# Kernel optimization log

Hardware: AMD Instinct MI355X
Metric: run time of the kernel (lower is better)

Reference implementation:

```python
import jax, jax.numpy as jnp
import numpy as np

NIN, NOUT = 256, 64

def setup_inputs() -> dict:
    key = jax.random.key(0)
    k1, k2, k3, k4 = jax.random.split(key, 4)
    B, T = 4, 4096
    y = jax.random.normal(k1, (B, T, NIN), dtype=jnp.float32)
    # torch Linear(nin, nout).weight has shape [nout, nin]; store as [nin, nout]
    s = 1.0 / np.sqrt(NIN)
    Wq = jax.random.uniform(k2, (NIN, NOUT), jnp.float32, -s, s)
    Wk = jax.random.uniform(k3, (NIN, NOUT), jnp.float32, -s, s)
    Wv = jax.random.uniform(k4, (NIN, NOUT), jnp.float32, -s, s)
    return {"y": y, "Wq": Wq, "Wk": Wk, "Wv": Wv}

def reference(y, Wq, Wk, Wv):
    T = y.shape[1]
    que = y @ Wq  # [B,T,NOUT]
    key = y @ Wk
    val = y @ Wv
    att = jnp.einsum('bqd,bkd->bqk', que, key)  # [B,T,T]
    causal = jnp.tril(jnp.ones((T, T), dtype=bool))  # True = keep
    att = jnp.where(causal, att, -jnp.inf)
    att = jax.nn.softmax(att / jnp.sqrt(jnp.float32(NOUT)), axis=-1)
    return jnp.einsum('bqk,bkd->bqd', att, val)
```

## Files before the change

### kernel.cpp

```cpp
#include <hip/hip_runtime.h>
#include <hip/hip_bf16.h>

#define TLEN 4096
#define NINP 256
#define DD   64

#define QSCALE 0.18033688011112042f

typedef __attribute__((ext_vector_type(8))) short bf16x8;
typedef __attribute__((ext_vector_type(4))) short bf16x4;
typedef __attribute__((ext_vector_type(4))) float f32x4;

union U8 { bf16x8 v; uint u[4]; };
union U4 { bf16x4 v; uint u[2]; };

__device__ inline ushort bfu(float x) {
    union { float f; uint u; } a; a.f = x;
    uint r = a.u + 0x7fffu + ((a.u >> 16) & 1u);
    return (ushort)(r >> 16);
}
__device__ inline uint pk2(float lo, float hi) {
    return (uint)bfu(lo) | ((uint)bfu(hi) << 16);
}
__device__ inline uint cvtpk(float lo, float hi) {
    uint r;
    asm("v_cvt_pk_bf16_f32 %0, %1, %2" : "=v"(r) : "v"(lo), "v"(hi));
    return r;
}

__device__ inline bf16x8 ld16(const ushort* p) {
    return *(const bf16x8*)p;
}
__device__ inline bf16x8 ld8x2(const ushort* p) {
    U8 u;
    uint2 a = *(const uint2*)p;
    uint2 b = *(const uint2*)(p + 4);
    u.u[0] = a.x; u.u[1] = a.y; u.u[2] = b.x; u.u[3] = b.y;
    return u.v;
}

__global__ __launch_bounds__(256) void prep_wt(
    const float* __restrict__ Wq, const float* __restrict__ Wk,
    const float* __restrict__ Wv, ushort* __restrict__ WT)
{
    __shared__ ushort lt[256 * 66];
    const int t = threadIdx.x;
    const int m = blockIdx.x;
    const float* W = (m == 0) ? Wq : ((m == 1) ? Wk : Wv);
    const float scale = (m == 0) ? QSCALE : 1.0f;

    #pragma unroll
    for (int j = 0; j < 16; ++j) {
        int i4 = t + 256 * j;
        float4 v = *(const float4*)&W[i4 * 4];
        int k = i4 >> 4, d = (i4 * 4) & 63;
        *(uint*)&lt[k * 66 + d]     = pk2(v.x * scale, v.y * scale);
        *(uint*)&lt[k * 66 + d + 2] = pk2(v.z * scale, v.w * scale);
    }
    __syncthreads();
    #pragma unroll
    for (int j = 0; j < 32; ++j) {
        int o2 = t + 256 * j;
        int d = o2 >> 7, k = (o2 & 127) * 2;
        uint pk = (uint)lt[k * 66 + d] | ((uint)lt[(k + 1) * 66 + d] << 16);
        *(uint*)&WT[m * 16384 + d * 256 + k] = pk;
    }
}

__global__ __launch_bounds__(256, 3) void qkv_kernel(
    const float* __restrict__ y, const ushort* __restrict__ WT,
    ushort* __restrict__ Qh, ushort* __restrict__ Kp, ushort* __restrict__ Vp,
    const int rbn)
{
    __shared__ ushort Wl[64 * 268];
    __shared__ ushort tb[64 * 68];

    const int t = threadIdx.x;
    const int w = t >> 6, lane = t & 63;
    const int quad = lane >> 4, l15 = lane & 15;
    const int mb = blockIdx.x / rbn;
    const int rb = blockIdx.x % rbn;
    const int rowbase = rb * 64;
    const int myrow = rowbase + w * 16 + l15;

    {
        int n = t >> 2, seg = t & 3;
        const ushort* src = WT + mb * 16384 + n * 256 + seg * 64;
        ushort* dst = &Wl[n * 268 + seg * 64];
        #pragma unroll
        for (int j = 0; j < 16; ++j)
            ((uint2*)dst)[j] = ((const uint2*)src)[j];
    }

    bf16x8 afrag[8];
    const float* yrow = y + (size_t)myrow * NINP;
    #pragma unroll
    for (int s = 0; s < 8; ++s) {
        float4 lo = *(const float4*)&yrow[s * 32 + quad * 8];
        float4 hi = *(const float4*)&yrow[s * 32 + quad * 8 + 4];
        U8 u;
        u.u[0] = pk2(lo.x, lo.y);
        u.u[1] = pk2(lo.z, lo.w);
        u.u[2] = pk2(hi.x, hi.y);
        u.u[3] = pk2(hi.z, hi.w);
        afrag[s] = u.v;
    }

    __syncthreads();

    f32x4 acc[4];
    #pragma unroll
    for (int nt = 0; nt < 4; ++nt) acc[nt] = f32x4{0.f, 0.f, 0.f, 0.f};

    #pragma unroll
    for (int s = 0; s < 8; ++s)
        #pragma unroll
        for (int nt = 0; nt < 4; ++nt) {
            bf16x8 bfrag = ld8x2(&Wl[(nt * 16 + l15) * 268 + s * 32 + quad * 8]);
            acc[nt] = __builtin_amdgcn_mfma_f32_16x16x32_bf16(
                afrag[s], bfrag, acc[nt], 0, 0, 0);
        }

    if (mb == 0) {
        #pragma unroll
        for (int nt = 0; nt < 4; ++nt)
            #pragma unroll
            for (int r = 0; r < 4; ++r)
                tb[(w * 16 + quad * 4 + r) * 68 + nt * 16 + l15] = bfu(acc[nt][r]);
        __syncthreads();
        int row = t >> 2, seg = t & 3;
        ushort* gd = Qh + (size_t)(rowbase + row) * DD + seg * 16;
        const ushort* sp = &tb[row * 68 + seg * 16];
        #pragma unroll
        for (int j = 0; j < 4; ++j) ((uint2*)gd)[j] = ((const uint2*)sp)[j];
    } else if (mb == 1) {
        #pragma unroll
        for (int nt = 0; nt < 4; ++nt)
            #pragma unroll
            for (int r = 0; r < 4; ++r)
                tb[(w * 16 + quad * 4 + r) * 68 + nt * 16 + l15] = bfu(acc[nt][r]);
        __syncthreads();
        #pragma unroll
        for (int j = 0; j < 2; ++j) {
            int idx = t + 256 * j;
            int instr = idx >> 6, ln = idx & 63;
            int kt = instr >> 1, s = instr & 1;
            int q2 = ln >> 4, l15b = ln & 15;
            int row = kt * 16 + l15b, dcol = s * 32 + q2 * 8;
            const ushort* sp = &tb[row * 68 + dcol];
            ushort* gd = Kp + (size_t)rb * 4096 + idx * 8;
            ((uint2*)gd)[0] = ((const uint2*)sp)[0];
            ((uint2*)gd)[1] = ((const uint2*)sp)[1];
        }
    } else {
        #pragma unroll
        for (int nt = 0; nt < 4; ++nt) {
            int d = nt * 16 + l15;
            #pragma unroll
            for (int r = 0; r < 4; r += 2) {
                int tt = w * 16 + quad * 4 + r;
                *(uint*)&tb[d * 68 + tt] = pk2(acc[nt][r], acc[nt][r + 1]);
            }
        }
        __syncthreads();
        #pragma unroll
        for (int j = 0; j < 2; ++j) {
            int idx = t + 256 * j;
            int instr = idx >> 6, ln = idx & 63;
            int nt = instr >> 1, m = instr & 1;
            int q2 = ln >> 4, l15b = ln & 15;
            int d = nt * 16 + l15b;
            int k0 = 32 * m + q2 * 4;
            ushort* gd = Vp + (size_t)rb * 4096 + idx * 8;
            ((uint2*)gd)[0] = *(const uint2*)&tb[d * 68 + k0];
            ((uint2*)gd)[1] = *(const uint2*)&tb[d * 68 + k0 + 16];
        }
    }
}

__device__ inline void load_k32(bf16x8 (&kf)[2][2], const ushort* __restrict__ Kw,
                                int ci)
{
    const ushort* base = Kw + (size_t)ci * 2048;
    #pragma unroll
    for (int kt = 0; kt < 2; ++kt)
        #pragma unroll
        for (int s = 0; s < 2; ++s)
            kf[kt][s] = ld16(base + (kt * 2 + s) * 512);
}

__device__ inline void load_v32(U4 (&vt)[4][2], const ushort* __restrict__ Vw,
                                int ci)
{
    const ushort* base = Vw + (size_t)(ci >> 1) * 4096 + (ci & 1) * 512;
    #pragma unroll
    for (int nt = 0; nt < 4; ++nt) {
        U8 uu; uu.v = ld16(base + nt * 1024);
        vt[nt][0].u[0] = uu.u[0]; vt[nt][0].u[1] = uu.u[1];
        vt[nt][1].u[0] = uu.u[2]; vt[nt][1].u[1] = uu.u[3];
    }
}

__global__ __launch_bounds__(768, 2) void attn_kernel(
    const ushort* __restrict__ Qh, const ushort* __restrict__ Kp,
    const ushort* __restrict__ Vp, float* __restrict__ out)
{
    __shared__ float Ob[12][32 * 68];
    __shared__ float lb[12][32];

    const int t = threadIdx.x;
    const int w = t >> 6, lane = t & 63;
    const int quad = lane >> 4, l15 = lane & 15;

    const int x  = blockIdx.x & 7;
    const int b  = x >> 1;
    const int pr = (((int)blockIdx.x >> 3) << 1) | (x & 1);

    const ushort* Qb = Qh + (size_t)b * TLEN * DD;
    const ushort* Kw = Kp + (size_t)b * 64 * 4096 + lane * 8;
    const ushort* Vw = Vp + (size_t)b * 64 * 4096 + lane * 8;
    float* outb = out + (size_t)b * TLEN * DD;

    for (int half = 0; half < 2; ++half) {
        const int tile = half ? (127 - pr) : pr;
        const int seg  = half ? (11 - w) : w;
        const int qb   = tile * 32;
        const int nc   = tile + 1;
        const int cps  = (nc + 11) / 12;
        const int clo  = seg * cps;
        const int chi  = (nc < clo + cps) ? nc : (clo + cps);

        f32x4 oT[2][4];
        #pragma unroll
        for (int qt = 0; qt < 2; ++qt)
            #pragma unroll
            for (int nt = 0; nt < 4; ++nt)
                oT[qt][nt] = f32x4{0.f, 0.f, 0.f, 0.f};
        float l_acc[2] = {0.f, 0.f};

        if (clo < chi) {
            bf16x8 qf[2][2];
            #pragma unroll
            for (int qt = 0; qt < 2; ++qt)
                #pragma unroll
                for (int s = 0; s < 2; ++s)
                    qf[qt][s] = ld16(Qb + (size_t)(qb + qt * 16 + l15) * DD + s * 32 + quad * 8);

            bf16x8 kf[2][2];
            load_k32(kf, Kw, clo);

            for (int ci = clo; ci < chi; ++ci) {
                const int c0 = ci * 32;

                U4 vt[4][2];
                load_v32(vt, Vw, ci);

                f32x4 st[2][2];
                #pragma unroll
                for (int qt = 0; qt < 2; ++qt)
                    #pragma unroll
                    for (int kt = 0; kt < 2; ++kt)
                        st[qt][kt] = f32x4{0.f, 0.f, 0.f, 0.f};
                __builtin_amdgcn_s_setprio(1);
                #pragma unroll
                for (int s = 0; s < 2; ++s)
                    #pragma unroll
                    for (int qt = 0; qt < 2; ++qt)
                        #pragma unroll
                        for (int kt = 0; kt < 2; ++kt)
                            st[qt][kt] = __builtin_amdgcn_mfma_f32_16x16x32_bf16(
                                kf[kt][s], qf[qt][s], st[qt][kt], 0, 0, 0);
                __builtin_amdgcn_s_setprio(0);

                if (ci + 1 < chi) load_k32(kf, Kw, ci + 1);

                U4 pa[2][2];
                if (c0 + 31 <= qb) {
                    #pragma unroll
                    for (int qt = 0; qt < 2; ++qt)
                        #pragma unroll
                        for (int kt = 0; kt < 2; ++kt) {
                            float p0 = exp2f(st[qt][kt][0]);
                            float p1 = exp2f(st[qt][kt][1]);
                            float p2 = exp2f(st[qt][kt][2]);
                            float p3 = exp2f(st[qt][kt][3]);
                            l_acc[qt] += (p0 + p1) + (p2 + p3);
                            pa[qt][kt].u[0] = cvtpk(p0, p1);
                            pa[qt][kt].u[1] = cvtpk(p2, p3);
                        }
                } else {
                    #pragma unroll
                    for (int qt = 0; qt < 2; ++qt) {
                        const int q = qb + qt * 16 + l15;
                        #pragma unroll
                        for (int kt = 0; kt < 2; ++kt) {
                            const int kb0 = c0 + kt * 16 + quad * 4;
                            float p[4];
                            #pragma unroll
                            for (int r = 0; r < 4; ++r) {
                                float e = exp2f(st[qt][kt][r]);
                                p[r] = (kb0 + r <= q) ? e : 0.f;
                                l_acc[qt] += p[r];
                            }
                            pa[qt][kt].u[0] = cvtpk(p[0], p[1]);
                            pa[qt][kt].u[1] = cvtpk(p[2], p[3]);
                        }
                    }
                }

                __builtin_amdgcn_s_setprio(1);
                #pragma unroll
                for (int qt = 0; qt < 2; ++qt)
                    #pragma unroll
                    for (int nt = 0; nt < 4; ++nt)
                        #pragma unroll
                        for (int kt = 0; kt < 2; ++kt)
                            oT[qt][nt] = __builtin_amdgcn_mfma_f32_16x16x16bf16_1k(
                                vt[nt][kt].v, pa[qt][kt].v, oT[qt][nt], 0, 0, 0);
                __builtin_amdgcn_s_setprio(0);
            }

            #pragma unroll
            for (int qt = 0; qt < 2; ++qt) {
                l_acc[qt] += __shfl_xor(l_acc[qt], 16, 64);
                l_acc[qt] += __shfl_xor(l_acc[qt], 32, 64);
            }
        }

        #pragma unroll
        for (int qt = 0; qt < 2; ++qt) {
            #pragma unroll
            for (int nt = 0; nt < 4; ++nt)
                #pragma unroll
                for (int r = 0; r < 4; ++r)
                    Ob[w][(qt * 16 + l15) * 68 + nt * 16 + quad * 4 + r] = oT[qt][nt][r];
            if (quad == 0) lb[w][qt * 16 + l15] = l_acc[qt];
        }
        __syncthreads();

        #pragma unroll
        for (int e = 0; e < 3; ++e) {
            int idx = t + 768 * e;
            if (idx < 2048) {
                int q = idx >> 6, d = idx & 63;
                float s = 0.f, ls = 0.f;
                #pragma unroll
                for (int ww = 0; ww < 12; ++ww) {
                    s += Ob[ww][q * 68 + d];
                    ls += lb[ww][q];
                }
                outb[(size_t)(qb + q) * DD + d] = s * __builtin_amdgcn_rcpf(ls);
            }
        }
        __syncthreads();
    }
}

extern "C" void kernel_launch(void* const* d_in, const int* in_sizes, int n_in,
                              void* d_out, int out_size, void* d_ws, size_t ws_size,
                              hipStream_t stream) {
    const float* y  = (const float*)d_in[0];
    const float* Wq = (const float*)d_in[1];
    const float* Wk = (const float*)d_in[2];
    const float* Wv = (const float*)d_in[3];
    float* outp = (float*)d_out;

    const int rows = in_sizes[0] / NINP;
    const int nb = rows / TLEN;
    const int rbn = rows / 64;

    ushort* WT = (ushort*)d_ws;
    ushort* Qh = WT + 3 * 16384;
    ushort* Kp = Qh + (size_t)rows * DD;
    ushort* Vp = Kp + (size_t)rows * DD;

    prep_wt<<<3, 256, 0, stream>>>(Wq, Wk, Wv, WT);
    qkv_kernel<<<3 * rbn, 256, 0, stream>>>(y, WT, Qh, Kp, Vp, rbn);
    attn_kernel<<<nb * 64, 768, 0, stream>>>(Qh, Kp, Vp, outp);
}
```

Baseline: 101.4 us.

## Prefetch K two chunks ahead and load QKV weights pre-swizzled from global

prep_wt now writes the projection weights directly in MFMA B-fragment order. qkv_kernel can therefore load each fragment with one 16-byte global read, dropping the LDS staging buffer and its barrier. The attention inner loop is split into a helper that alternates two K register buffers, prefetching K two chunks ahead to hide load latency. The attention launch bound is raised to 3 blocks per CU. That caps registers more tightly and may cause spills, while the LDS footprint likely still allows only two resident blocks.

New measurement: 101.1 us, median of 2. Within noise of the previous version (-0.3%).

```diff
diff --git a/kernel.cpp b/kernel.cpp
--- a/kernel.cpp
+++ b/kernel.cpp
@@ -31,17 +31,10 @@
 __device__ inline bf16x8 ld16(const ushort* p) {
     return *(const bf16x8*)p;
 }
-__device__ inline bf16x8 ld8x2(const ushort* p) {
-    U8 u;
-    uint2 a = *(const uint2*)p;
-    uint2 b = *(const uint2*)(p + 4);
-    u.u[0] = a.x; u.u[1] = a.y; u.u[2] = b.x; u.u[3] = b.y;
-    return u.v;
-}
 
 __global__ __launch_bounds__(256) void prep_wt(
     const float* __restrict__ Wq, const float* __restrict__ Wk,
-    const float* __restrict__ Wv, ushort* __restrict__ WT)
+    const float* __restrict__ Wv, ushort* __restrict__ WTf)
 {
     __shared__ ushort lt[256 * 66];
     const int t = threadIdx.x;
@@ -59,20 +52,27 @@
     }
     __syncthreads();
     #pragma unroll
-    for (int j = 0; j < 32; ++j) {
-        int o2 = t + 256 * j;
-        int d = o2 >> 7, k = (o2 & 127) * 2;
-        uint pk = (uint)lt[k * 66 + d] | ((uint)lt[(k + 1) * 66 + d] << 16);
-        *(uint*)&WT[m * 16384 + d * 256 + k] = pk;
-    }
-}
-
-__global__ __launch_bounds__(256, 3) void qkv_kernel(
-    const float* __restrict__ y, const ushort* __restrict__ WT,
+    for (int j = 0; j < 8; ++j) {
+        int slot = t + 256 * j;
+        int u = slot >> 6, ln = slot & 63;
+        int s = u >> 2, nt = u & 3;
+        int d = nt * 16 + (ln & 15);
+        int k0 = s * 32 + (ln >> 4) * 8;
+        uint a0 = (uint)lt[(k0 + 0) * 66 + d] | ((uint)lt[(k0 + 1) * 66 + d] << 16);
+        uint a1 = (uint)lt[(k0 + 2) * 66 + d] | ((uint)lt[(k0 + 3) * 66 + d] << 16);
+        uint a2 = (uint)lt[(k0 + 4) * 66 + d] | ((uint)lt[(k0 + 5) * 66 + d] << 16);
+        uint a3 = (uint)lt[(k0 + 6) * 66 + d] | ((uint)lt[(k0 + 7) * 66 + d] << 16);
+        ushort* gd = WTf + m * 16384 + slot * 8;
+        ((uint2*)gd)[0] = uint2{a0, a1};
+        ((uint2*)gd)[1] = uint2{a2, a3};
+    }
+}
+
+__global__ __launch_bounds__(256) void qkv_kernel(
+    const float* __restrict__ y, const ushort* __restrict__ WTf,
     ushort* __restrict__ Qh, ushort* __restrict__ Kp, ushort* __restrict__ Vp,
     const int rbn)
 {
-    __shared__ ushort Wl[64 * 268];
     __shared__ ushort tb[64 * 68];
 
     const int t = threadIdx.x;
@@ -82,15 +82,6 @@
     const int rb = blockIdx.x % rbn;
     const int rowbase = rb * 64;
     const int myrow = rowbase + w * 16 + l15;
-
-    {
-        int n = t >> 2, seg = t & 3;
-        const ushort* src = WT + mb * 16384 + n * 256 + seg * 64;
-        ushort* dst = &Wl[n * 268 + seg * 64];
-        #pragma unroll
-        for (int j = 0; j < 16; ++j)
-            ((uint2*)dst)[j] = ((const uint2*)src)[j];
-    }
 
     bf16x8 afrag[8];
     const float* yrow = y + (size_t)myrow * NINP;
@@ -106,17 +97,16 @@
         afrag[s] = u.v;
     }
 
-    __syncthreads();
-
     f32x4 acc[4];
     #pragma unroll
     for (int nt = 0; nt < 4; ++nt) acc[nt] = f32x4{0.f, 0.f, 0.f, 0.f};
 
+    const ushort* Wm = WTf + mb * 16384 + lane * 8;
     #pragma unroll
     for (int s = 0; s < 8; ++s)
         #pragma unroll
         for (int nt = 0; nt < 4; ++nt) {
-            bf16x8 bfrag = ld8x2(&Wl[(nt * 16 + l15) * 268 + s * 32 + quad * 8]);
+            bf16x8 bfrag = ld16(Wm + (s * 4 + nt) * 512);
             acc[nt] = __builtin_amdgcn_mfma_f32_16x16x32_bf16(
                 afrag[s], bfrag, acc[nt], 0, 0, 0);
         }
@@ -201,7 +191,82 @@
     }
 }
 
-__global__ __launch_bounds__(768, 2) void attn_kernel(
+__device__ inline void chunk32(
+    const bf16x8 (&kf)[2][2], bf16x8 (&kfn)[2][2],
+    const ushort* __restrict__ Kw, const ushort* __restrict__ Vw,
+    const bf16x8 (&qf)[2][2], f32x4 (&oT)[2][4], float (&l_acc)[2],
+    int ci, int pf, int chi, int qb, int quad, int l15)
+{
+    const int c0 = ci * 32;
+    U4 vt[4][2];
+    load_v32(vt, Vw, ci);
+
+    f32x4 st[2][2];
+    #pragma unroll
+    for (int qt = 0; qt < 2; ++qt)
+        #pragma unroll
+        for (int kt = 0; kt < 2; ++kt)
+            st[qt][kt] = f32x4{0.f, 0.f, 0.f, 0.f};
+    __builtin_amdgcn_s_setprio(1);
+    #pragma unroll
+    for (int s = 0; s < 2; ++s)
+        #pragma unroll
+        for (int qt = 0; qt < 2; ++qt)
+            #pragma unroll
+            for (int kt = 0; kt < 2; ++kt)
+                st[qt][kt] = __builtin_amdgcn_mfma_f32_16x16x32_bf16(
+                    kf[kt][s], qf[qt][s], st[qt][kt], 0, 0, 0);
+    __builtin_amdgcn_s_setprio(0);
+
+    if (pf < chi) load_k32(kfn, Kw, pf);
+
+    U4 pa[2][2];
+    if (c0 + 31 <= qb) {
+        #pragma unroll
+        for (int qt = 0; qt < 2; ++qt)
+            #pragma unroll
+            for (int kt = 0; kt < 2; ++kt) {
+                float p0 = exp2f(st[qt][kt][0]);
+                float p1 = exp2f(st[qt][kt][1]);
+                float p2 = exp2f(st[qt][kt][2]);
+                float p3 = exp2f(st[qt][kt][3]);
+                l_acc[qt] += (p0 + p1) + (p2 + p3);
+                pa[qt][kt].u[0] = cvtpk(p0, p1);
+                pa[qt][kt].u[1] = cvtpk(p2, p3);
+            }
+    } else {
+        #pragma unroll
+        for (int qt = 0; qt < 2; ++qt) {
+            const int q = qb + qt * 16 + l15;
+            #pragma unroll
+            for (int kt = 0; kt < 2; ++kt) {
+                const int kb0 = c0 + kt * 16 + quad * 4;
+                float p[4];
+                #pragma unroll
+                for (int r = 0; r < 4; ++r) {
+                    float e = exp2f(st[qt][kt][r]);
+                    p[r] = (kb0 + r <= q) ? e : 0.f;
+                    l_acc[qt] += p[r];
+                }
+                pa[qt][kt].u[0] = cvtpk(p[0], p[1]);
+                pa[qt][kt].u[1] = cvtpk(p[2], p[3]);
+            }
+        }
+    }
+
+    __builtin_amdgcn_s_setprio(1);
+    #pragma unroll
+    for (int qt = 0; qt < 2; ++qt)
+        #pragma unroll
+        for (int nt = 0; nt < 4; ++nt)
+            #pragma unroll
+            for (int kt = 0; kt < 2; ++kt)
+                oT[qt][nt] = __builtin_amdgcn_mfma_f32_16x16x16bf16_1k(
+                    vt[nt][kt].v, pa[qt][kt].v, oT[qt][nt], 0, 0, 0);
+    __builtin_amdgcn_s_setprio(0);
+}
+
+__global__ __launch_bounds__(768, 3) void attn_kernel(
     const ushort* __restrict__ Qh, const ushort* __restrict__ Kp,
     const ushort* __restrict__ Vp, float* __restrict__ out)
 {
@@ -246,78 +311,16 @@
                 for (int s = 0; s < 2; ++s)
                     qf[qt][s] = ld16(Qb + (size_t)(qb + qt * 16 + l15) * DD + s * 32 + quad * 8);
 
-            bf16x8 kf[2][2];
-            load_k32(kf, Kw, clo);
-
-            for (int ci = clo; ci < chi; ++ci) {
-                const int c0 = ci * 32;
-
-                U4 vt[4][2];
-                load_v32(vt, Vw, ci);
-
-                f32x4 st[2][2];
-                #pragma unroll
-                for (int qt = 0; qt < 2; ++qt)
-                    #pragma unroll
-                    for (int kt = 0; kt < 2; ++kt)
-                        st[qt][kt] = f32x4{0.f, 0.f, 0.f, 0.f};
-                __builtin_amdgcn_s_setprio(1);
-                #pragma unroll
-                for (int s = 0; s < 2; ++s)
-                    #pragma unroll
-                    for (int qt = 0; qt < 2; ++qt)
-                        #pragma unroll
-                        for (int kt = 0; kt < 2; ++kt)
-                            st[qt][kt] = __builtin_amdgcn_mfma_f32_16x16x32_bf16(
-                                kf[kt][s], qf[qt][s], st[qt][kt], 0, 0, 0);
-                __builtin_amdgcn_s_setprio(0);
-
-                if (ci + 1 < chi) load_k32(kf, Kw, ci + 1);
-
-                U4 pa[2][2];
-                if (c0 + 31 <= qb) {
-                    #pragma unroll
-                    for (int qt = 0; qt < 2; ++qt)
-                        #pragma unroll
-                        for (int kt = 0; kt < 2; ++kt) {
-                            float p0 = exp2f(st[qt][kt][0]);
-                            float p1 = exp2f(st[qt][kt][1]);
-                            float p2 = exp2f(st[qt][kt][2]);
-                            float p3 = exp2f(st[qt][kt][3]);
-                            l_acc[qt] += (p0 + p1) + (p2 + p3);
-                            pa[qt][kt].u[0] = cvtpk(p0, p1);
-                            pa[qt][kt].u[1] = cvtpk(p2, p3);
-                        }
-                } else {
-                    #pragma unroll
-                    for (int qt = 0; qt < 2; ++qt) {
-                        const int q = qb + qt * 16 + l15;
-                        #pragma unroll
-                        for (int kt = 0; kt < 2; ++kt) {
-                            const int kb0 = c0 + kt * 16 + quad * 4;
-                            float p[4];
-                            #pragma unroll
-                            for (int r = 0; r < 4; ++r) {
-                                float e = exp2f(st[qt][kt][r]);
-                                p[r] = (kb0 + r <= q) ? e : 0.f;
-                                l_acc[qt] += p[r];
-                            }
-                            pa[qt][kt].u[0] = cvtpk(p[0], p[1]);
-                            pa[qt][kt].u[1] = cvtpk(p[2], p[3]);
-                        }
-                    }
-                }
-
-                __builtin_amdgcn_s_setprio(1);
-                #pragma unroll
-                for (int qt = 0; qt < 2; ++qt)
-                    #pragma unroll
-                    for (int nt = 0; nt < 4; ++nt)
-                        #pragma unroll
-                        for (int kt = 0; kt < 2; ++kt)
-                            oT[qt][nt] = __builtin_amdgcn_mfma_f32_16x16x16bf16_1k(
-                                vt[nt][kt].v, pa[qt][kt].v, oT[qt][nt], 0, 0, 0);
-                __builtin_amdgcn_s_setprio(0);
+            bf16x8 kfA[2][2], kfB[2][2];
+            load_k32(kfA, Kw, clo);
+            if (clo + 1 < chi) load_k32(kfB, Kw, clo + 1);
+
+            for (int ci = clo; ci < chi; ci += 2) {
+                chunk32(kfA, kfA, Kw, Vw, qf, oT, l_acc,
+                        ci, ci + 2, chi, qb, quad, l15);
+                if (ci + 1 < chi)
+                    chunk32(kfB, kfB, Kw, Vw, qf, oT, l_acc,
+                            ci + 1, ci + 3, chi, qb, quad, l15);
             }
 
             #pragma unroll
```
